# Kernel optimization log

Measured on AMD Instinct MI355X. Metric: run time of the kernel, lower is better.

The kernel has to match this reference:

```python
import jax, jax.numpy as jnp
import numpy as np
from math import comb

B = 1024                 # num_batch
NUM, NVAR, NUM_OBS = 100, 11, 10
T_FIN = 15.0
K_P = 20.0; K_D = 2.0 * np.sqrt(20.0); K_P_V = 20.0
A_OBS, B_OBS = 8.0, 4.2
RHO_V, RHO_PROJ, RHO_LANE, RHO_OBS, RHO_OFFSET, RHO_INEQ = 1.0, 1.0, 100.0, 100.0, 1.0, 100.0
V_MIN, V_MAX, A_MAX = 0.1, 30.0, 8.0
MAXITER = 20
LATENT, HID, INP_DIM, TRAJ_DIM = 2, 1024, 55, 200


def _bernstein():
    # degree-10 Bernstein polynomial basis on [0, T_FIN], sampled at NUM points
    n = NVAR - 1
    s = np.linspace(0.0, 1.0, NUM)
    bm = lambda m: np.stack([comb(m, k) * s**k * (1.0 - s)**(m - k) for k in range(m + 1)], 1)
    P, B9, B8 = bm(n), bm(n - 1), bm(n - 2)
    Z = np.zeros(NUM)
    Pdot = np.stack([(n / T_FIN) * ((B9[:, k - 1] if k >= 1 else Z) - (B9[:, k] if k <= n - 1 else Z)) for k in range(n + 1)], 1)
    Pddot = np.stack([(n * (n - 1) / T_FIN**2) * ((B8[:, k - 2] if k >= 2 else Z) - 2.0 * (B8[:, k - 1] if 1 <= k <= n - 1 else Z) + (B8[:, k] if k <= n - 2 else Z)) for k in range(n + 1)], 1)
    return tuple(jnp.asarray(a, jnp.float32) for a in (P, Pdot, Pddot))


def _forward(inp, initial_state_ego, traj_gt, y_ub, y_lb, eps,
             enc_w1, enc_b1, enc_w2, enc_b2, enc_wmu, enc_bmu, enc_wlv, enc_blv,
             dec_w1, dec_b1, dec_w2, dec_b2, dec_w3, dec_b3,
             P, Pdot, Pddot, inp_mean, inp_std):
    Bn = inp.shape[0]
    tot_time = jnp.linspace(0.0, T_FIN, NUM)

    # ---- cVAE encode / reparameterize / decode ----
    inp_n = (inp - inp_mean) / inp_std
    h = jax.nn.relu(jnp.concatenate([inp_n, traj_gt], 1) @ enc_w1 + enc_b1)
    h = jax.nn.relu(h @ enc_w2 + enc_b2)
    mu = h @ enc_wmu + enc_bmu
    logvar = h @ enc_wlv + enc_blv
    z = mu + jnp.exp(0.5 * logvar) * eps
    h = jax.nn.relu(jnp.concatenate([z, inp_n], 1) @ dec_w1 + dec_b1)
    h = jax.nn.relu(h @ dec_w2 + dec_b2)
    nn_out = h @ dec_w3 + dec_b3          # (B, 8): 4 v_des + 4 y_des setpoints

    # ---- constant constraint matrices ----
    A_eq_x = jnp.stack([P[0], Pdot[0], Pddot[0]])                 # (3, 11)
    A_eq_y = jnp.stack([P[0], Pdot[0], Pddot[0], Pdot[-1]])       # (4, 11)
    A_pd = Pddot - K_P * P - K_D * Pdot
    A_vd = Pddot - K_P_V * Pdot
    cost_smooth = Pddot.T @ Pddot
    I = jnp.eye(NVAR, dtype=P.dtype)

    def kkt_inv(cost, A_eq):
        m = A_eq.shape[0]
        M = jnp.block([[cost, A_eq.T], [A_eq, jnp.zeros((m, m), cost.dtype)]])
        return jnp.linalg.inv(M)

    # ---- boundary conditions ----
    zb = jnp.zeros((Bn,), inp.dtype)
    b_eq_x = jnp.stack([zb, initial_state_ego[:, 2], zb], 1)
    b_eq_y = jnp.stack([zb, initial_state_ego[:, 3], zb, zb], 1)

    # ---- QP layer 1 (behavioral layer) ----
    # sum_i A_vd_i^T A_vd_i over the 4 row-partitions == A_vd^T A_vd
    cost1_x = cost_smooth + RHO_V * (A_vd.T @ A_vd)
    cost1_y = cost_smooth + RHO_OFFSET * (A_pd.T @ A_pd)
    inv1_x = kkt_inv(cost1_x, A_eq_x)
    inv1_y = kkt_inv(cost1_y, A_eq_y)
    v_des = jnp.repeat(nn_out[:, 0:4], NUM // 4, axis=1)   # (B, 100) piecewise setpoints
    y_des = jnp.repeat(nn_out[:, 4:8], NUM // 4, axis=1)
    lincost_x1 = -RHO_V * ((-K_P_V * v_des) @ A_vd)
    lincost_y1 = -RHO_OFFSET * ((-K_P * y_des) @ A_pd)
    c_x_bar = (jnp.concatenate([-lincost_x1, b_eq_x], 1) @ inv1_x.T)[:, :NVAR]
    c_y_bar = (jnp.concatenate([-lincost_y1, b_eq_y], 1) @ inv1_y.T)[:, :NVAR]

    # ---- obstacle constant-velocity rollouts (obstacle-major, matches tile(P)) ----
    x_obs, y_obs = inp[:, 5::5], inp[:, 6::5]
    vx_obs, vy_obs = inp[:, 7::5], inp[:, 8::5]
    x_obs_traj = (x_obs[:, :, None] + vx_obs[:, :, None] * tot_time).reshape(Bn, NUM_OBS * NUM)
    y_obs_traj = (y_obs[:, :, None] + vy_obs[:, :, None] * tot_time).reshape(Bn, NUM_OBS * NUM)

    # ---- QP layer 2 (iterative ADMM-style projection) ----
    A_obs_m = jnp.tile(P, (NUM_OBS, 1))          # (1000, 11)
    A_lane = jnp.vstack([P, -P])                 # (200, 11)
    A_vel, A_acc = Pdot, Pddot
    cost2_x = RHO_PROJ * I + RHO_OBS * (A_obs_m.T @ A_obs_m) + RHO_INEQ * (A_acc.T @ A_acc) + RHO_INEQ * (A_vel.T @ A_vel)
    cost2_y = cost2_x + RHO_LANE * (A_lane.T @ A_lane)
    inv2_x = kkt_inv(cost2_x, A_eq_x)
    inv2_y = kkt_inv(cost2_y, A_eq_y)
    ones_num = jnp.ones((1, NUM), inp.dtype)
    b_lane = jnp.concatenate([y_ub[:, None] * ones_num, -y_lb[:, None] * ones_num], 1)  # (B, 200)

    def step(carry, _):
        primal, lx, ly = carry
        cx, cy = primal[:, :NVAR], primal[:, NVAR:]
        x, xdot, xddot = cx @ P.T, cx @ Pdot.T, cx @ Pddot.T
        y, ydot, yddot = cy @ P.T, cy @ Pdot.T, cy @ Pddot.T
        # obstacle polar decomposition
        wc = jnp.tile(x, (1, NUM_OBS)) - x_obs_traj
        ws = jnp.tile(y, (1, NUM_OBS)) - y_obs_traj
        a_o = jnp.arctan2(A_OBS * ws, B_OBS * wc)
        ca, sa = jnp.cos(a_o), jnp.sin(a_o)
        c1 = RHO_OBS * (A_OBS**2 * ca**2 + B_OBS**2 * sa**2)
        c2 = RHO_OBS * (A_OBS * wc * ca + B_OBS * ws * sa)
        d_o = jnp.maximum(1.0, c2 / c1)
        # velocity / acceleration polar decomposition with box clipping
        a_v = jnp.arctan2(ydot, xdot)
        cv, sv = jnp.cos(a_v), jnp.sin(a_v)
        d_v = jnp.clip(xdot * cv + ydot * sv, V_MIN, V_MAX)
        a_a = jnp.arctan2(yddot, xddot)
        caa, saa = jnp.cos(a_a), jnp.sin(a_a)
        d_a = jnp.clip(xddot * caa + yddot * saa, 0.0, A_MAX)
        # lane slack
        lane_proj = cy @ A_lane.T
        s_lane = jnp.maximum(0.0, b_lane - lane_proj)
        res_lane = lane_proj - b_lane + s_lane
        # residuals -> dual updates
        rxo = wc - A_OBS * d_o * ca
        ryo = ws - B_OBS * d_o * sa
        rvx, rvy = xdot - d_v * cv, ydot - d_v * sv
        rax, ray = xddot - d_a * caa, yddot - d_a * saa
        lx = lx - RHO_OBS * (rxo @ A_obs_m) - RHO_INEQ * (rax @ A_acc) - RHO_INEQ * (rvx @ A_vel)
        ly = ly - RHO_OBS * (ryo @ A_obs_m) - RHO_INEQ * (ray @ A_acc) - RHO_INEQ * (rvy @ A_vel) - RHO_LANE * (res_lane @ A_lane)
        # linear cost + batched KKT solve via precomputed inverse
        b_ox = x_obs_traj + A_OBS * d_o * ca
        b_oy = y_obs_traj + B_OBS * d_o * sa
        lin_x = -lx - RHO_PROJ * c_x_bar - RHO_OBS * (b_ox @ A_obs_m) - RHO_INEQ * ((d_a * caa) @ A_acc) - RHO_INEQ * ((d_v * cv) @ A_vel)
        lin_y = -ly - RHO_PROJ * c_y_bar - RHO_OBS * (b_oy @ A_obs_m) - RHO_INEQ * ((d_a * saa) @ A_acc) - RHO_INEQ * ((d_v * sv) @ A_vel) - RHO_LANE * ((b_lane - s_lane) @ A_lane)
        sx = (jnp.concatenate([-lin_x, b_eq_x], 1) @ inv2_x.T)[:, :NVAR]
        sy = (jnp.concatenate([-lin_y, b_eq_y], 1) @ inv2_y.T)[:, :NVAR]
        return (jnp.concatenate([sx, sy], 1), lx, ly), None

    primal0 = jnp.concatenate([c_x_bar, c_y_bar], 1)
    lam0 = jnp.zeros((Bn, NVAR), inp.dtype)
    (primal, _, _), _ = jax.lax.scan(step, (primal0, lam0, lam0), None, length=MAXITER)
    return primal  # (B, 2*NVAR) projected trajectory coefficients


def setup_inputs() -> dict:
    key = jax.random.key(0)
    ks = jax.random.split(key, 16)
    P, Pdot, Pddot = _bernstein()
    n = lambda k, sh, sc=1.0: sc * jax.random.normal(k, sh, jnp.float32)
    return {
        "inp": n(ks[0], (B, INP_DIM), 5.0),
        "initial_state_ego": jnp.concatenate([jnp.zeros((B, 2), jnp.float32), 10.0 + n(ks[1], (B, 2))], 1),
        "traj_gt": n(ks[2], (B, TRAJ_DIM)),
        "y_ub": jnp.full((B,), 3.5, jnp.float32),
        "y_lb": jnp.full((B,), -3.5, jnp.float32),
        "eps": n(ks[3], (B, LATENT)),
        "enc_w1": n(ks[4], (INP_DIM + TRAJ_DIM, HID), 0.05), "enc_b1": jnp.zeros((HID,), jnp.float32),
        "enc_w2": n(ks[5], (HID, HID), 0.03), "enc_b2": jnp.zeros((HID,), jnp.float32),
        "enc_wmu": n(ks[6], (HID, LATENT), 0.03), "enc_bmu": jnp.zeros((LATENT,), jnp.float32),
        "enc_wlv": n(ks[7], (HID, LATENT), 0.03), "enc_blv": jnp.zeros((LATENT,), jnp.float32),
        "dec_w1": n(ks[8], (LATENT + INP_DIM, HID), 0.05), "dec_b1": jnp.zeros((HID,), jnp.float32),
        "dec_w2": n(ks[9], (HID, HID), 0.03), "dec_b2": jnp.zeros((HID,), jnp.float32),
        "dec_w3": n(ks[10], (HID, 8), 0.03), "dec_b3": jnp.zeros((8,), jnp.float32),
        "P": P, "Pdot": Pdot, "Pddot": Pddot,
        "inp_mean": jnp.zeros((INP_DIM,), jnp.float32),
        "inp_std": jnp.ones((INP_DIM,), jnp.float32),
    }


def reference(inp, initial_state_ego, traj_gt, y_ub, y_lb, eps,
              enc_w1, enc_b1, enc_w2, enc_b2, enc_wmu, enc_bmu, enc_wlv, enc_blv,
              dec_w1, dec_b1, dec_w2, dec_b2, dec_w3, dec_b3,
              P, Pdot, Pddot, inp_mean, inp_std):
    return _forward(inp, initial_state_ego, traj_gt, y_ub, y_lb, eps,
                    enc_w1, enc_b1, enc_w2, enc_b2, enc_wmu, enc_bmu, enc_wlv, enc_blv,
                    dec_w1, dec_b1, dec_w2, dec_b2, dec_w3, dec_b3,
                    P, Pdot, Pddot, inp_mean, inp_std)
```

## Files before the change

### kernel.cpp

```cpp
#include <hip/hip_runtime.h>
#include <hip/hip_bf16.h>
#include <math.h>

#define BATCH   1024
#define NUMPT   100
#define NVAR    11
#define NOBS    10
#define HID     1024
#define INPD    55
#define TRAJD   200

#define T_FIN_C   15.0f
#define K_P_C     20.0f
#define K_D_C     8.944271909999159f
#define K_P_V_C   20.0f
#define A_OBS_C   8.0f
#define B_OBS_C   4.2f
#define AB_C      33.6f
#define ABSQ_C    1128.96f
#define RHO_V_C      1.0f
#define RHO_PROJ_C   1.0f
#define RHO_LANE_C   100.0f
#define RHO_OBS_C    100.0f
#define RHO_OFFSET_C 1.0f
#define RHO_INEQ_C   100.0f
#define V_MIN_C   0.1f
#define V_MAX_C   30.0f
#define A_MAX_C   8.0f
#define MAXIT     20

#define WS_INV1X  0
#define WS_INV1Y  256
#define WS_INV2X  512
#define WS_INV2Y  768
#define WS_SVD    1024
#define WS_SPD    1088
#define WS_QX     1152
#define WS_QY     1280
#define WS_R2X    1408
#define WS_R2Y    1536
#define WS_BIG    2048

typedef __bf16 bf16x8 __attribute__((ext_vector_type(8)));
typedef float  f32x4  __attribute__((ext_vector_type(4)));

__global__ __launch_bounds__(256) void setup_kernel(
    const float* __restrict__ Pg, const float* __restrict__ Pdg,
    const float* __restrict__ Pddg, float* __restrict__ ws,
    const float* __restrict__ inp, const float* __restrict__ traj,
    const float* __restrict__ mean, const float* __restrict__ stdv,
    __bf16* __restrict__ enc_in, __bf16* __restrict__ dec_in,
    const float* __restrict__ w1, const float* __restrict__ w2,
    const float* __restrict__ w3, const float* __restrict__ w4,
    __bf16* __restrict__ o1, __bf16* __restrict__ o2,
    __bf16* __restrict__ o3, __bf16* __restrict__ o4)
{
    __shared__ float sP[NUMPT*NVAR], sPd[NUMPT*NVAR], sPdd[NUMPT*NVAR];
    __shared__ float aug[15][31];
    __shared__ float fcol[15];
    __shared__ float sQ[121];
    __shared__ float sn[INPD];
    __shared__ float s_pivinv;
    __shared__ int   s_pidx;
    const int tid = threadIdx.x, bid = blockIdx.x;

    if (bid >= 1028) {
        const int idx = (bid - 1028) * 256 + tid;
        if (idx < 262144) {
            const int n = idx >> 8, k = idx & 255;
            o1[idx] = (__bf16)((k < 255) ? w1[(size_t)k*HID + n] : 0.0f);
        } else if (idx < 262144 + 1048576) {
            const int i = idx - 262144;
            const int n = i >> 10, k = i & 1023;
            o2[i] = (__bf16)w2[(size_t)k*HID + n];
        } else if (idx < 262144 + 1048576 + 65536) {
            const int i = idx - (262144 + 1048576);
            const int n = i >> 6, k = i & 63;
            o3[i] = (__bf16)((k < 57) ? w3[(size_t)k*HID + n] : 0.0f);
        } else {
            const int i = idx - (262144 + 1048576 + 65536);
            const int n = i >> 10, k = i & 1023;
            o4[i] = (__bf16)w4[(size_t)k*HID + n];
        }
        return;
    }

    if (bid >= 4) {
        const int b = bid - 4;
        if (tid < INPD) {
            const float v = (inp[b*INPD + tid] - mean[tid]) / stdv[tid];
            sn[tid] = v;
            enc_in[b*256 + tid] = (__bf16)v;
        } else if (tid < 255) {
            enc_in[b*256 + tid] = (__bf16)traj[b*TRAJD + (tid - INPD)];
        } else {
            enc_in[b*256 + 255] = (__bf16)0.0f;
        }
        __syncthreads();
        if (tid >= 2 && tid < 64)
            dec_in[b*64 + tid] = (__bf16)((tid < 57) ? sn[tid - 2] : 0.0f);
        return;
    }

    for (int i = tid; i < NUMPT*NVAR; i += 256) {
        sP[i] = Pg[i]; sPd[i] = Pdg[i]; sPdd[i] = Pddg[i];
    }
    for (int i = tid; i < 15*31; i += 256) (&aug[0][0])[i] = 0.0f;
    __syncthreads();

    const int N = (bid == 0 || bid == 2) ? 14 : 15;

    if (tid < 121) {
        const int i = tid / 11, j = tid % 11;
        float s = 0.0f;
        if (bid == 0) {
            for (int t = 0; t < NUMPT; ++t) {
                float pdd_i = sPdd[t*NVAR+i], pdd_j = sPdd[t*NVAR+j];
                float av_i = pdd_i - K_P_V_C * sPd[t*NVAR+i];
                float av_j = pdd_j - K_P_V_C * sPd[t*NVAR+j];
                s += pdd_i*pdd_j + RHO_V_C * av_i*av_j;
            }
        } else if (bid == 1) {
            for (int t = 0; t < NUMPT; ++t) {
                float pdd_i = sPdd[t*NVAR+i], pdd_j = sPdd[t*NVAR+j];
                float ap_i = pdd_i - K_P_C*sP[t*NVAR+i] - K_D_C*sPd[t*NVAR+i];
                float ap_j = pdd_j - K_P_C*sP[t*NVAR+j] - K_D_C*sPd[t*NVAR+j];
                s += pdd_i*pdd_j + RHO_OFFSET_C * ap_i*ap_j;
            }
        } else {
            float obs_w = RHO_OBS_C * (float)NOBS;
            if (bid == 3) obs_w += RHO_LANE_C * 2.0f;
            for (int t = 0; t < NUMPT; ++t) {
                float p_i = sP[t*NVAR+i],   p_j = sP[t*NVAR+j];
// ... 48 lines not shown
        const int p = s_pidx;
        if (p != k && tid < 2*N) {
            float tmp = aug[k][tid]; aug[k][tid] = aug[p][tid]; aug[p][tid] = tmp;
        }
        __syncthreads();
        if (tid == 0) s_pivinv = 1.0f / aug[k][k];
        __syncthreads();
        if (tid < 2*N) aug[k][tid] *= s_pivinv;
        __syncthreads();
        if (tid < N) fcol[tid] = (tid == k) ? 0.0f : aug[tid][k];
        __syncthreads();
        for (int idx = tid; idx < N*2*N; idx += 256) {
            const int i = idx / (2*N), j = idx % (2*N);
            if (i != k) aug[i][j] = fmaf(-fcol[i], aug[k][j], aug[i][j]);
        }
        __syncthreads();
    }

    float* dst = ws + (bid == 0 ? WS_INV1X : bid == 1 ? WS_INV1Y
                      : bid == 2 ? WS_INV2X : WS_INV2Y);
    for (int idx = tid; idx < N*N; idx += 256)
        dst[idx] = aug[idx / N][N + idx % N];
    __syncthreads();

    if ((bid == 2 || bid == 3) && tid < 121) {
        const int k = tid / 11, j = tid % 11;
        float a = 0.0f;
        #pragma unroll
        for (int m = 0; m < 11; ++m) a = fmaf(aug[k][N + m], sQ[m*11 + j], a);
        ws[(bid == 2 ? WS_R2X : WS_R2Y) + tid] = a;
    }
}

__global__ __launch_bounds__(256) void gemm_mfma(
    const __bf16* __restrict__ A, const __bf16* __restrict__ Wt,
    const float* __restrict__ bias, __bf16* __restrict__ C, int Kp)
{
    __shared__ __bf16 As[32][72];
    __shared__ __bf16 Bs[64][72];
    const int tid = threadIdx.x;
    const int lane = tid & 63, wv = tid >> 6;
    const int wm = (wv >> 1) * 16, wn = (wv & 1) * 32;
    const int ln = lane & 15, q = lane >> 4;
    const int row0 = blockIdx.y * 32, col0 = blockIdx.x * 64;
    const int srow = tid >> 3, lc = (tid & 7) * 8;

    f32x4 acc0 = (f32x4){0,0,0,0}, acc1 = (f32x4){0,0,0,0};

    for (int k0 = 0; k0 < Kp; k0 += 64) {
        *(bf16x8*)&As[srow][lc] =
            *(const bf16x8*)&A[(size_t)(row0 + srow) * Kp + k0 + lc];
        *(bf16x8*)&Bs[srow][lc] =
            *(const bf16x8*)&Wt[(size_t)(col0 + srow) * Kp + k0 + lc];
        *(bf16x8*)&Bs[srow + 32][lc] =
            *(const bf16x8*)&Wt[(size_t)(col0 + srow + 32) * Kp + k0 + lc];
        __syncthreads();
        #pragma unroll
        for (int kc = 0; kc < 2; ++kc) {
            const bf16x8 a  = *(const bf16x8*)&As[wm + ln][kc*32 + q*8];
            const bf16x8 b0 = *(const bf16x8*)&Bs[wn + ln][kc*32 + q*8];
            const bf16x8 b1 = *(const bf16x8*)&Bs[wn + 16 + ln][kc*32 + q*8];
            acc0 = __builtin_amdgcn_mfma_f32_16x16x32_bf16(a, b0, acc0, 0, 0, 0);
            acc1 = __builtin_amdgcn_mfma_f32_16x16x32_bf16(a, b1, acc1, 0, 0, 0);
        }
        __syncthreads();
    }
    #pragma unroll
    for (int ni = 0; ni < 2; ++ni) {
        const int col = col0 + wn + ni*16 + ln;
        const float bv = bias[col];
        const f32x4 av = ni ? acc1 : acc0;
        #pragma unroll
        for (int r = 0; r < 4; ++r) {
            const int row = row0 + wm + q*4 + r;
            C[(size_t)row * HID + col] = (__bf16)fmaxf(av[r] + bv, 0.0f);
        }
    }
}

__global__ __launch_bounds__(64) void z_kernel(
    const __bf16* __restrict__ h, const float* __restrict__ wmu,
    const float* __restrict__ bmu, const float* __restrict__ wlv,
    const float* __restrict__ blv, const float* __restrict__ eps,
    __bf16* __restrict__ dec_in)
{
    const int b = blockIdx.x, lane = threadIdx.x;
    float a0 = 0, a1 = 0, a2 = 0, a3 = 0;
    for (int hh = lane; hh < HID; hh += 64) {
        const float v = (float)h[b*HID + hh];
        a0 = fmaf(v, wmu[hh*2 + 0], a0);
        a1 = fmaf(v, wmu[hh*2 + 1], a1);
        a2 = fmaf(v, wlv[hh*2 + 0], a2);
        a3 = fmaf(v, wlv[hh*2 + 1], a3);
    }
    #pragma unroll
    for (int off = 32; off; off >>= 1) {
        a0 += __shfl_down(a0, off);
        a1 += __shfl_down(a1, off);
        a2 += __shfl_down(a2, off);
        a3 += __shfl_down(a3, off);
    }
    if (lane == 0) {
        const float mu0 = a0 + bmu[0], mu1 = a1 + bmu[1];
        const float lv0 = a2 + blv[0], lv1 = a3 + blv[1];
        dec_in[b*64 + 0] = (__bf16)fmaf(expf(0.5f*lv0), eps[b*2 + 0], mu0);
        dec_in[b*64 + 1] = (__bf16)fmaf(expf(0.5f*lv1), eps[b*2 + 1], mu1);
    }
}

__global__ __launch_bounds__(64) void out8_kernel(
    const __bf16* __restrict__ h, const float* __restrict__ w3,
    const float* __restrict__ b3, float* __restrict__ nn_out)
{
    const int b = blockIdx.x, lane = threadIdx.x;
    float acc[8] = {};
    for (int hh = lane; hh < HID; hh += 64) {
        const float v = (float)h[b*HID + hh];
        #pragma unroll
        for (int j = 0; j < 8; ++j) acc[j] = fmaf(v, w3[hh*8 + j], acc[j]);
    }
    #pragma unroll
    for (int j = 0; j < 8; ++j)
        #pragma unroll
        for (int off = 32; off; off >>= 1) acc[j] += __shfl_down(acc[j], off);
    if (lane == 0)
        for (int j = 0; j < 8; ++j) nn_out[b*8 + j] = acc[j] + b3[j];
}

#define DOT11(bb, a0, a1, a2) \
    fmaf(bb[0],a0.x, fmaf(bb[1],a0.y, fmaf(bb[2],a0.z, fmaf(bb[3],a0.w, \
    fmaf(bb[4],a1.x, fmaf(bb[5],a1.y, fmaf(bb[6],a1.z, fmaf(bb[7],a1.w, \
    fmaf(bb[8],a2.x, fmaf(bb[9],a2.y, bb[10]*a2.z))))))))))

__global__ __launch_bounds__(256) void solver_kernel(
    const float* __restrict__ nn_out, const float* __restrict__ inp,
    const float* __restrict__ ise, const float* __restrict__ yub_p,
    const float* __restrict__ ylb_p,
    const float* __restrict__ Pg, const float* __restrict__ Pdg,
    const float* __restrict__ Pddg,
    const float* __restrict__ ws, float* __restrict__ out)
{
    __shared__ __align__(16) float sBcol[3][11][108];
    __shared__ float s_i2x[196], s_i2y[225], sR2x[121], sR2y[121];
    __shared__ __align__(16) float rows[7][104];
    __shared__ float dval[2][80];
    __shared__ __align__(16) float cxs[12], cys[12];
    __shared__ float wlin[24];
    __shared__ float obsS[4][10];

    const int tid = threadIdx.x;
    const int e = blockIdx.x;

    for (int i = tid; i < 3*11*108; i += 256) {
        const int mat = i / 1188, rem = i - mat*1188;
        const int k = rem / 108, t = rem - k*108;
        const float* G = (mat == 0) ? Pg : (mat == 1 ? Pdg : Pddg);
        sBcol[mat][k][t] = (t < NUMPT) ? G[t*NVAR + k] : 0.0f;
    }
    for (int i = tid; i < 196; i += 256) s_i2x[i] = ws[WS_INV2X + i];
    for (int i = tid; i < 225; i += 256) s_i2y[i] = ws[WS_INV2Y + i];
    for (int i = tid; i < 121; i += 256) { sR2x[i] = ws[WS_R2X + i]; sR2y[i] = ws[WS_R2Y + i]; }
    if (tid >= 200 && tid < 240) {
        const int i = tid - 200;
        obsS[i/10][i%10] = inp[e*INPD + 5 + (i/10) + 5*(i%10)];
    }
    if (tid >= 64 && tid < 92) {
        const int i = tid - 64;
        rows[i >> 2][100 + (i & 3)] = 0.0f;
    }
    if (tid == 92) cxs[11] = 0.0f;
    if (tid == 93) cys[11] = 0.0f;

    const bool isA = (tid < 200);
    const int tA = tid >> 1, hA = tid & 1;
    const bool isB = (tid < 154);
    const int hB = (tid >= 77) ? 1 : 0;
    const int dB = tid - 77*hB;
    const int rB = dB / 11, kB = dB - 11*rB;
    const int mB = (rB==1||rB==4) ? 2 : ((rB==2||rB==5) ? 1 : 0);
    const float* colp = &sBcol[mB][kB][hB*52];
    const float* rowp = &rows[rB][hB*52];

    float bP[NVAR], bQ[NVAR];
    if (isA) {
        const float* Qsrc = hA ? Pddg : Pdg;
        #pragma unroll
        for (int k = 0; k < NVAR; ++k) {
            bP[k] = Pg[tA*NVAR+k];
            bQ[k] = Qsrc[tA*NVAR+k];
        }
    }

    const float vx0 = ise[e*4 + 2], vy0 = ise[e*4 + 3];
    const float yub = yub_p[e], ylb = ylb_p[e];
    __syncthreads();

    const float DT = T_FIN_C / 99.0f;
    float xo[5], yo[5];
    if (isA) {
        const int ob0 = 5*hA;
        #pragma unroll
        for (int o = 0; o < 5; ++o) {
            xo[o] = fmaf(obsS[2][ob0+o], tA*DT, obsS[0][ob0+o]);
            yo[o] = fmaf(obsS[3][ob0+o], tA*DT, obsS[1][ob0+o]);
        }
    }

    if (tid < 11) {
        float s = 0;
        #pragma unroll
        for (int c = 0; c < 4; ++c)
            s = fmaf(nn_out[e*8 + c], ws[WS_SVD + c*11 + tid], s);
        wlin[tid] = RHO_V_C * K_P_V_C * s;
    } else if (tid < 22) {
        const int k = tid - 11;
        float s = 0;
        #pragma unroll
        for (int c = 0; c < 4; ++c)
            s = fmaf(nn_out[e*8 + 4 + c], ws[WS_SPD + c*11 + k], s);
        wlin[tid] = RHO_OFFSET_C * K_P_C * s;
    }
    __syncthreads();
// ... 45 lines not shown
            }
            const float mrx = srx + __shfl_xor(srx, 1);
            const float mry = sry + __shfl_xor(sry, 1);

            if (hA == 0) {
                rows[0][tA] = mrx;
                rows[3][tA] = mry;
                const float rv2 = qx*qx + qy*qy;
                float vxr, vyr;
                if (rv2 > 0.0f) {
                    const float ri = rsqrtf(rv2);
                    const float dv = fminf(fmaxf(rv2*ri, V_MIN_C), V_MAX_C);
                    const float f = 1.0f - dv*ri;
                    vxr = qx*f; vyr = qy*f;
                } else { vxr = -V_MIN_C; vyr = 0.0f; }
                rows[2][tA] = vxr;  rows[5][tA] = vyr;
                rows[6][tA] = fmaxf(0.0f, py - yub) - fmaxf(0.0f, ylb - py);
            } else {
                const float ra2 = qx*qx + qy*qy;
                float axr = 0.0f, ayr = 0.0f;
                if (ra2 > A_MAX_C*A_MAX_C) {
                    const float ri = rsqrtf(ra2);
                    const float f = 1.0f - A_MAX_C*ri;
                    axr = qx*f; ayr = qy*f;
                }
                rows[1][tA] = axr;  rows[4][tA] = ayr;
            }
        }
        __syncthreads();

        if (isB) {
            float s0 = 0.0f, s1 = 0.0f;
            #pragma unroll
            for (int i = 0; i < 13; ++i) {
                const float4 rr = *(const float4*)&rowp[i*4];
                const float4 cc = *(const float4*)&colp[i*4];
                s0 = fmaf(rr.x, cc.x, s0); s1 = fmaf(rr.y, cc.y, s1);
                s0 = fmaf(rr.z, cc.z, s0); s1 = fmaf(rr.w, cc.w, s1);
            }
            dval[hB][dB] = s0 + s1;
        }
        __syncthreads();

        if (tid < 22) {
            const int k = (tid < 11) ? tid : tid - 11;
            float u;
            if (tid < 11)
                u = RHO_OBS_C * ((dval[0][k]      + dval[1][k])
                               + (dval[0][11 + k] + dval[1][11 + k])
                               + (dval[0][22 + k] + dval[1][22 + k]));
            else
                u = RHO_OBS_C * ((dval[0][33 + k] + dval[1][33 + k])
                               + (dval[0][44 + k] + dval[1][44 + k])
                               + (dval[0][55 + k] + dval[1][55 + k])
                               + (dval[0][66 + k] + dval[1][66 + k]));
            wlin[tid] = 2.0f*u - lam - cb;
            lam -= u;
        }
        __builtin_amdgcn_wave_barrier();
        if (tid < 22) {
            const int k = (tid < 11) ? tid : tid - 11;
            if (tid < 11) {
                float a = vx0 * s_i2x[k*14 + 12];
                #pragma unroll
                for (int j = 0; j < NVAR; ++j) {
                    a = fmaf(-wlin[j], s_i2x[k*14 + j], a);
                    a = fmaf(sR2x[k*11 + j], cxs[j], a);
                }
                cxs[k] = a;
            } else {
                float a = vy0 * s_i2y[k*15 + 12];
                #pragma unroll
                for (int j = 0; j < NVAR; ++j) {
                    a = fmaf(-wlin[11 + j], s_i2y[k*15 + j], a);
                    a = fmaf(sR2y[k*11 + j], cys[j], a);
                }
                cys[k] = a;
            }
        }
        __syncthreads();
    }

    if (tid < NVAR) {
        out[e*22 + tid]      = cxs[tid];
        out[e*22 + 11 + tid] = cys[tid];
    }
}

extern "C" void kernel_launch(void* const* d_in, const int* in_sizes, int n_in,
                              void* d_out, int out_size, void* d_ws, size_t ws_size,
                              hipStream_t stream)
{
    (void)in_sizes; (void)n_in; (void)out_size; (void)ws_size;
    const float* inp    = (const float*)d_in[0];
    const float* ise    = (const float*)d_in[1];
    const float* traj   = (const float*)d_in[2];
    const float* yub    = (const float*)d_in[3];
    const float* ylb    = (const float*)d_in[4];
    const float* eps    = (const float*)d_in[5];
    const float* enc_w1 = (const float*)d_in[6];
    const float* enc_b1 = (const float*)d_in[7];
    const float* enc_w2 = (const float*)d_in[8];
    const float* enc_b2 = (const float*)d_in[9];
    const float* wmu    = (const float*)d_in[10];
    const float* bmu    = (const float*)d_in[11];
    const float* wlv    = (const float*)d_in[12];
    const float* blv    = (const float*)d_in[13];
    const float* dec_w1 = (const float*)d_in[14];
    const float* dec_b1 = (const float*)d_in[15];
    const float* dec_w2 = (const float*)d_in[16];
    const float* dec_b2 = (const float*)d_in[17];
    const float* dec_w3 = (const float*)d_in[18];
    const float* dec_b3 = (const float*)d_in[19];
    const float* P      = (const float*)d_in[20];
    const float* Pd     = (const float*)d_in[21];
    const float* Pdd    = (const float*)d_in[22];
    const float* mean   = (const float*)d_in[23];
    const float* stdv   = (const float*)d_in[24];

    float* ws   = (float*)d_ws;
    float* nn   = ws + WS_BIG;
    __bf16* bfb = (__bf16*)(ws + WS_BIG + BATCH*8);
    __bf16* enc_in = bfb;
    __bf16* dec_in = enc_in + (size_t)BATCH*256;
    __bf16* hA     = dec_in + (size_t)BATCH*64;
    __bf16* hB     = hA + (size_t)BATCH*HID;
    __bf16* wt1    = hB + (size_t)BATCH*HID;
    __bf16* wt2    = wt1 + (size_t)HID*256;
    __bf16* wt3    = wt2 + (size_t)HID*HID;
    __bf16* wt4    = wt3 + (size_t)HID*64;
    float* outf = (float*)d_out;

    setup_kernel<<<4 + 1024 + 9472, 256, 0, stream>>>(
        P, Pd, Pdd, ws, inp, traj, mean, stdv, enc_in, dec_in,
        enc_w1, enc_w2, dec_w1, dec_w2, wt1, wt2, wt3, wt4);

    dim3 g(16, 32);
    gemm_mfma<<<g, 256, 0, stream>>>(enc_in, wt1, enc_b1, hA, 256);
    gemm_mfma<<<g, 256, 0, stream>>>(hA, wt2, enc_b2, hB, 1024);
    z_kernel<<<BATCH, 64, 0, stream>>>(hB, wmu, bmu, wlv, blv, eps, dec_in);
    gemm_mfma<<<g, 256, 0, stream>>>(dec_in, wt3, dec_b1, hA, 64);
    gemm_mfma<<<g, 256, 0, stream>>>(hA, wt4, dec_b2, hB, 1024);
    out8_kernel<<<BATCH, 64, 0, stream>>>(hB, dec_w3, dec_b3, nn);

    solver_kernel<<<BATCH, 256, 0, stream>>>(nn, inp, ise, yub, ylb,
                                             P, Pd, Pdd, ws, outf);
}
```

Measured before the change: 236.6 us.

## Widen GEMM K-tile to 128 and keep solver basis columns in registers

The MFMA GEMM now stages 128-wide K slices per iteration instead of 64, which halves the number of barrier-separated loop trips. To keep that tile size valid, the decoder-input K dimension is padded from 64 to 128. The solver kernel drops its shared-memory Bernstein column table and holds each thread's 36-element column slice in registers. The 11x7 dot products are now split across 231 threads in three chunks instead of 154 threads in two, and launch_bounds adds an occupancy hint of 4 blocks. In exchange, the decoder's first GEMM does extra padded-K work, and the solver's register footprint grows.

```diff
diff --git a/kernel.cpp b/kernel.cpp
--- a/kernel.cpp
+++ b/kernel.cpp
@@ -43,6 +43,12 @@
 
 typedef __bf16 bf16x8 __attribute__((ext_vector_type(8)));
 typedef float  f32x4  __attribute__((ext_vector_type(4)));
+
+#define CV1  262144
+#define CV2  1048576
+#define CV3  131072
+#define CV4  1048576
+#define CVTOT (CV1 + CV2 + CV3 + CV4)
 
 __global__ __launch_bounds__(256) void setup_kernel(
     const float* __restrict__ Pg, const float* __restrict__ Pdg,
@@ -66,19 +72,19 @@
 
     if (bid >= 1028) {
         const int idx = (bid - 1028) * 256 + tid;
-        if (idx < 262144) {
+        if (idx < CV1) {
             const int n = idx >> 8, k = idx & 255;
             o1[idx] = (__bf16)((k < 255) ? w1[(size_t)k*HID + n] : 0.0f);
-        } else if (idx < 262144 + 1048576) {
-            const int i = idx - 262144;
+        } else if (idx < CV1 + CV2) {
+            const int i = idx - CV1;
             const int n = i >> 10, k = i & 1023;
             o2[i] = (__bf16)w2[(size_t)k*HID + n];
-        } else if (idx < 262144 + 1048576 + 65536) {
-            const int i = idx - (262144 + 1048576);
-            const int n = i >> 6, k = i & 63;
+        } else if (idx < CV1 + CV2 + CV3) {
+            const int i = idx - (CV1 + CV2);
+            const int n = i >> 7, k = i & 127;
             o3[i] = (__bf16)((k < 57) ? w3[(size_t)k*HID + n] : 0.0f);
         } else {
-            const int i = idx - (262144 + 1048576 + 65536);
+            const int i = idx - (CV1 + CV2 + CV3);
             const int n = i >> 10, k = i & 1023;
             o4[i] = (__bf16)w4[(size_t)k*HID + n];
         }
@@ -97,8 +103,8 @@
             enc_in[b*256 + 255] = (__bf16)0.0f;
         }
         __syncthreads();
-        if (tid >= 2 && tid < 64)
-            dec_in[b*64 + tid] = (__bf16)((tid < 57) ? sn[tid - 2] : 0.0f);
+        if (tid >= 2 && tid < 128)
+            dec_in[b*128 + tid] = (__bf16)((tid < 57) ? sn[tid - 2] : 0.0f);
         return;
     }
 
@@ -217,27 +223,29 @@
     const __bf16* __restrict__ A, const __bf16* __restrict__ Wt,
     const float* __restrict__ bias, __bf16* __restrict__ C, int Kp)
 {
-    __shared__ __bf16 As[32][72];
-    __shared__ __bf16 Bs[64][72];
+    __shared__ __bf16 As[32][136];
+    __shared__ __bf16 Bs[64][136];
     const int tid = threadIdx.x;
     const int lane = tid & 63, wv = tid >> 6;
     const int wm = (wv >> 1) * 16, wn = (wv & 1) * 32;
     const int ln = lane & 15, q = lane >> 4;
     const int row0 = blockIdx.y * 32, col0 = blockIdx.x * 64;
-    const int srow = tid >> 3, lc = (tid & 7) * 8;
+    const int r16 = tid >> 4, ch = (tid & 15) * 8;
 
     f32x4 acc0 = (f32x4){0,0,0,0}, acc1 = (f32x4){0,0,0,0};
 
-    for (int k0 = 0; k0 < Kp; k0 += 64) {
-        *(bf16x8*)&As[srow][lc] =
-            *(const bf16x8*)&A[(size_t)(row0 + srow) * Kp + k0 + lc];
-        *(bf16x8*)&Bs[srow][lc] =
-            *(const bf16x8*)&Wt[(size_t)(col0 + srow) * Kp + k0 + lc];
-        *(bf16x8*)&Bs[srow + 32][lc] =
-            *(const bf16x8*)&Wt[(size_t)(col0 + srow + 32) * Kp + k0 + lc];
-        __syncthreads();
-        #pragma unroll
-        for (int kc = 0; kc < 2; ++kc) {
+    for (int k0 = 0; k0 < Kp; k0 += 128) {
+        *(bf16x8*)&As[r16][ch] =
+            *(const bf16x8*)&A[(size_t)(row0 + r16) * Kp + k0 + ch];
+        *(bf16x8*)&As[r16 + 16][ch] =
+            *(const bf16x8*)&A[(size_t)(row0 + r16 + 16) * Kp + k0 + ch];
+        #pragma unroll
+        for (int p = 0; p < 4; ++p)
+            *(bf16x8*)&Bs[r16 + 16*p][ch] =
+                *(const bf16x8*)&Wt[(size_t)(col0 + r16 + 16*p) * Kp + k0 + ch];
+        __syncthreads();
+        #pragma unroll
+        for (int kc = 0; kc < 4; ++kc) {
             const bf16x8 a  = *(const bf16x8*)&As[wm + ln][kc*32 + q*8];
             const bf16x8 b0 = *(const bf16x8*)&Bs[wn + ln][kc*32 + q*8];
             const bf16x8 b1 = *(const bf16x8*)&Bs[wn + 16 + ln][kc*32 + q*8];
@@ -284,8 +292,8 @@
     if (lane == 0) {
         const float mu0 = a0 + bmu[0], mu1 = a1 + bmu[1];
         const float lv0 = a2 + blv[0], lv1 = a3 + blv[1];
-        dec_in[b*64 + 0] = (__bf16)fmaf(expf(0.5f*lv0), eps[b*2 + 0], mu0);
-        dec_in[b*64 + 1] = (__bf16)fmaf(expf(0.5f*lv1), eps[b*2 + 1], mu1);
+        dec_in[b*128 + 0] = (__bf16)fmaf(expf(0.5f*lv0), eps[b*2 + 0], mu0);
+        dec_in[b*128 + 1] = (__bf16)fmaf(expf(0.5f*lv1), eps[b*2 + 1], mu1);
     }
 }
 
@@ -313,7 +321,7 @@
     fmaf(bb[4],a1.x, fmaf(bb[5],a1.y, fmaf(bb[6],a1.z, fmaf(bb[7],a1.w, \
     fmaf(bb[8],a2.x, fmaf(bb[9],a2.y, bb[10]*a2.z))))))))))
 
-__global__ __launch_bounds__(256) void solver_kernel(
+__global__ __launch_bounds__(256, 4) void solver_kernel(
     const float* __restrict__ nn_out, const float* __restrict__ inp,
     const float* __restrict__ ise, const float* __restrict__ yub_p,
     const float* __restrict__ ylb_p,
@@ -321,10 +329,9 @@
     const float* __restrict__ Pddg,
     const float* __restrict__ ws, float* __restrict__ out)
 {
-    __shared__ __align__(16) float sBcol[3][11][108];
     __shared__ float s_i2x[196], s_i2y[225], sR2x[121], sR2y[121];
-    __shared__ __align__(16) float rows[7][104];
-    __shared__ float dval[2][80];
+    __shared__ __align__(16) float rows[7][108];
+    __shared__ float dval[3][80];
     __shared__ __align__(16) float cxs[12], cys[12];
     __shared__ float wlin[24];
     __shared__ float obsS[4][10];
@@ -332,35 +339,28 @@
     const int tid = threadIdx.x;
     const int e = blockIdx.x;
 
-    for (int i = tid; i < 3*11*108; i += 256) {
-        const int mat = i / 1188, rem = i - mat*1188;
-        const int k = rem / 108, t = rem - k*108;
-        const float* G = (mat == 0) ? Pg : (mat == 1 ? Pdg : Pddg);
-        sBcol[mat][k][t] = (t < NUMPT) ? G[t*NVAR + k] : 0.0f;
-    }
     for (int i = tid; i < 196; i += 256) s_i2x[i] = ws[WS_INV2X + i];
     for (int i = tid; i < 225; i += 256) s_i2y[i] = ws[WS_INV2Y + i];
     for (int i = tid; i < 121; i += 256) { sR2x[i] = ws[WS_R2X + i]; sR2y[i] = ws[WS_R2Y + i]; }
+    if (tid >= 232 && tid < 240) {  }
     if (tid >= 200 && tid < 240) {
         const int i = tid - 200;
         obsS[i/10][i%10] = inp[e*INPD + 5 + (i/10) + 5*(i%10)];
     }
-    if (tid >= 64 && tid < 92) {
+    if (tid >= 64 && tid < 120) {
         const int i = tid - 64;
-        rows[i >> 2][100 + (i & 3)] = 0.0f;
-    }
-    if (tid == 92) cxs[11] = 0.0f;
-    if (tid == 93) cys[11] = 0.0f;
+        rows[i >> 3][100 + (i & 7)] = 0.0f;
+    }
+    if (tid == 120) cxs[11] = 0.0f;
+    if (tid == 121) cys[11] = 0.0f;
 
     const bool isA = (tid < 200);
     const int tA = tid >> 1, hA = tid & 1;
-    const bool isB = (tid < 154);
-    const int hB = (tid >= 77) ? 1 : 0;
+    const bool isB = (tid < 231);
+    const int hB = (tid >= 154) ? 2 : ((tid >= 77) ? 1 : 0);
     const int dB = tid - 77*hB;
     const int rB = dB / 11, kB = dB - 11*rB;
-    const int mB = (rB==1||rB==4) ? 2 : ((rB==2||rB==5) ? 1 : 0);
-    const float* colp = &sBcol[mB][kB][hB*52];
-    const float* rowp = &rows[rB][hB*52];
+    const float* rowp = &rows[rB][hB*36];
 
     float bP[NVAR], bQ[NVAR];
     if (isA) {
@@ -369,6 +369,20 @@
         for (int k = 0; k < NVAR; ++k) {
             bP[k] = Pg[tA*NVAR+k];
             bQ[k] = Qsrc[tA*NVAR+k];
+        }
+    }
+    float4 bc[9];
+    if (isB) {
+        const float* G = (rB==1||rB==4) ? Pddg : ((rB==2||rB==5) ? Pdg : Pg);
+        #pragma unroll
+        for (int i = 0; i < 9; ++i) {
+            const int t0 = hB*36 + i*4;
+            float4 v;
+            v.x = (t0+0 < NUMPT) ? G[(t0+0)*NVAR + kB] : 0.0f;
+            v.y = (t0+1 < NUMPT) ? G[(t0+1)*NVAR + kB] : 0.0f;
+            v.z = (t0+2 < NUMPT) ? G[(t0+2)*NVAR + kB] : 0.0f;
+            v.w = (t0+3 < NUMPT) ? G[(t0+3)*NVAR + kB] : 0.0f;
+            bc[i] = v;
         }
     }
 
@@ -480,11 +494,10 @@
         if (isB) {
             float s0 = 0.0f, s1 = 0.0f;
             #pragma unroll
-            for (int i = 0; i < 13; ++i) {
+            for (int i = 0; i < 9; ++i) {
                 const float4 rr = *(const float4*)&rowp[i*4];
-                const float4 cc = *(const float4*)&colp[i*4];
-                s0 = fmaf(rr.x, cc.x, s0); s1 = fmaf(rr.y, cc.y, s1);
-                s0 = fmaf(rr.z, cc.z, s0); s1 = fmaf(rr.w, cc.w, s1);
+                s0 = fmaf(rr.x, bc[i].x, s0); s1 = fmaf(rr.y, bc[i].y, s1);
+                s0 = fmaf(rr.z, bc[i].z, s0); s1 = fmaf(rr.w, bc[i].w, s1);
             }
             dval[hB][dB] = s0 + s1;
         }
@@ -494,14 +507,14 @@
             const int k = (tid < 11) ? tid : tid - 11;
             float u;
             if (tid < 11)
-                u = RHO_OBS_C * ((dval[0][k]      + dval[1][k])
-                               + (dval[0][11 + k] + dval[1][11 + k])
-                               + (dval[0][22 + k] + dval[1][22 + k]));
+                u = RHO_OBS_C * ((dval[0][k]      + dval[1][k]      + dval[2][k])
+                               + (dval[0][11 + k] + dval[1][11 + k] + dval[2][11 + k])
+                               + (dval[0][22 + k] + dval[1][22 + k] + dval[2][22 + k]));
             else
-                u = RHO_OBS_C * ((dval[0][33 + k] + dval[1][33 + k])
-                               + (dval[0][44 + k] + dval[1][44 + k])
-                               + (dval[0][55 + k] + dval[1][55 + k])
-                               + (dval[0][66 + k] + dval[1][66 + k]));
+                u = RHO_OBS_C * ((dval[0][33 + k] + dval[1][33 + k] + dval[2][33 + k])
+                               + (dval[0][44 + k] + dval[1][44 + k] + dval[2][44 + k])
+                               + (dval[0][55 + k] + dval[1][55 + k] + dval[2][55 + k])
+                               + (dval[0][66 + k] + dval[1][66 + k] + dval[2][66 + k]));
             wlin[tid] = 2.0f*u - lam - cb;
             lam -= u;
         }
@@ -571,15 +584,15 @@
     __bf16* bfb = (__bf16*)(ws + WS_BIG + BATCH*8);
     __bf16* enc_in = bfb;
     __bf16* dec_in = enc_in + (size_t)BATCH*256;
-    __bf16* hA     = dec_in + (size_t)BATCH*64;
+    __bf16* hA     = dec_in + (size_t)BATCH*128;
     __bf16* hB     = hA + (size_t)BATCH*HID;
     __bf16* wt1    = hB + (size_t)BATCH*HID;
     __bf16* wt2    = wt1 + (size_t)HID*256;
     __bf16* wt3    = wt2 + (size_t)HID*HID;
-    __bf16* wt4    = wt3 + (size_t)HID*64;
+    __bf16* wt4    = wt3 + (size_t)HID*128;
     float* outf = (float*)d_out;
 
-    setup_kernel<<<4 + 1024 + 9472, 256, 0, stream>>>(
+    setup_kernel<<<4 + 1024 + 9728, 256, 0, stream>>>(
         P, Pd, Pdd, ws, inp, traj, mean, stdv, enc_in, dec_in,
         enc_w1, enc_w2, dec_w1, dec_w2, wt1, wt2, wt3, wt4);
 
@@ -587,7 +600,7 @@
     gemm_mfma<<<g, 256, 0, stream>>>(enc_in, wt1, enc_b1, hA, 256);
     gemm_mfma<<<g, 256, 0, stream>>>(hA, wt2, enc_b2, hB, 1024);
     z_kernel<<<BATCH, 64, 0, stream>>>(hB, wmu, bmu, wlv, blv, eps, dec_in);
-    gemm_mfma<<<g, 256, 0, stream>>>(dec_in, wt3, dec_b1, hA, 64);
+    gemm_mfma<<<g, 256, 0, stream>>>(dec_in, wt3, dec_b1, hA, 128);
     gemm_mfma<<<g, 256, 0, stream>>>(hA, wt4, dec_b2, hB, 1024);
     out8_kernel<<<BATCH, 64, 0, stream>>>(hB, dec_w3, dec_b3, nn);
 
```

Result: no change. 238.2 us (+0.7%).

## Fuse latent and output projections into GEMM epilogues, tile weight transposes

Applied to the files above, without the earlier changes.

Folds the mu/logvar projection and the 8-wide output head into the epilogues of the preceding MFMA GEMMs. Per-tile partial sums are reduced with warp shuffles and atomically added into buffers zeroed or bias-initialized in setup. The reparameterization step moves into the A-tile load of the first decoder GEMM. Weight transposition now goes through 64x64 shared-memory tiles for coalesced reads and writes, and the GEMM K-step grows from 64 to 128. This removes two kernel launches and an intermediate activation round trip, at the cost of float atomics that make summation order nondeterministic.

```diff
diff --git a/kernel.cpp b/kernel.cpp
--- a/kernel.cpp
+++ b/kernel.cpp
@@ -53,34 +53,44 @@
     const float* __restrict__ w1, const float* __restrict__ w2,
     const float* __restrict__ w3, const float* __restrict__ w4,
     __bf16* __restrict__ o1, __bf16* __restrict__ o2,
-    __bf16* __restrict__ o3, __bf16* __restrict__ o4)
+    __bf16* __restrict__ o3, __bf16* __restrict__ o4,
+    float* __restrict__ nn, float* __restrict__ mulv,
+    const float* __restrict__ b3)
 {
     __shared__ float sP[NUMPT*NVAR], sPd[NUMPT*NVAR], sPdd[NUMPT*NVAR];
     __shared__ float aug[15][31];
     __shared__ float fcol[15];
     __shared__ float sQ[121];
     __shared__ float sn[INPD];
+    __shared__ float tile[64][65];
     __shared__ float s_pivinv;
     __shared__ int   s_pidx;
     const int tid = threadIdx.x, bid = blockIdx.x;
 
     if (bid >= 1028) {
-        const int idx = (bid - 1028) * 256 + tid;
-        if (idx < 262144) {
-            const int n = idx >> 8, k = idx & 255;
-            o1[idx] = (__bf16)((k < 255) ? w1[(size_t)k*HID + n] : 0.0f);
-        } else if (idx < 262144 + 1048576) {
-            const int i = idx - 262144;
-            const int n = i >> 10, k = i & 1023;
-            o2[i] = (__bf16)w2[(size_t)k*HID + n];
-        } else if (idx < 262144 + 1048576 + 65536) {
-            const int i = idx - (262144 + 1048576);
-            const int n = i >> 6, k = i & 63;
-            o3[i] = (__bf16)((k < 57) ? w3[(size_t)k*HID + n] : 0.0f);
-        } else {
-            const int i = idx - (262144 + 1048576 + 65536);
-            const int n = i >> 10, k = i & 1023;
-            o4[i] = (__bf16)w4[(size_t)k*HID + n];
+        const int tb = bid - 1028;
+        int wsel, kt, nt;
+        if (tb < 64)       { wsel = 0; kt = tb >> 4;        nt = tb & 15; }
+        else if (tb < 320) { wsel = 1; kt = (tb-64) >> 4;   nt = (tb-64) & 15; }
+        else if (tb < 352) { wsel = 2; kt = (tb-320) >> 4;  nt = (tb-320) & 15; }
+        else               { wsel = 3; kt = (tb-352) >> 4;  nt = (tb-352) & 15; }
+        const float* W = (wsel==0) ? w1 : (wsel==1) ? w2 : (wsel==2) ? w3 : w4;
+        __bf16* O      = (wsel==0) ? o1 : (wsel==1) ? o2 : (wsel==2) ? o3 : o4;
+        const int K  = (wsel==0) ? 255 : (wsel==2) ? 57 : 1024;
+        const int Kp = (wsel==0) ? 256 : (wsel==2) ? 128 : 1024;
+        if (kt*64 >= Kp) return;
+        const int k0 = kt*64, n0 = nt*64;
+        const int rr = tid >> 6, c = tid & 63;
+        #pragma unroll 4
+        for (int it = 0; it < 16; ++it) {
+            const int r = it*4 + rr;
+            tile[r][c] = (k0 + r < K) ? W[(size_t)(k0 + r)*HID + n0 + c] : 0.0f;
+        }
+        __syncthreads();
+        #pragma unroll 4
+        for (int it = 0; it < 16; ++it) {
+            const int r = it*4 + rr;
+            O[(size_t)(n0 + r)*Kp + k0 + c] = (__bf16)tile[c][r];
         }
         return;
     }
@@ -97,8 +107,10 @@
             enc_in[b*256 + 255] = (__bf16)0.0f;
         }
         __syncthreads();
-        if (tid >= 2 && tid < 64)
-            dec_in[b*64 + tid] = (__bf16)((tid < 57) ? sn[tid - 2] : 0.0f);
+        if (tid >= 2 && tid < 128)
+            dec_in[b*128 + tid] = (__bf16)((tid < 57) ? sn[tid - 2] : 0.0f);
+        if (tid < 4) mulv[b*4 + tid] = 0.0f;
+        else if (tid >= 8 && tid < 16) nn[b*8 + (tid - 8)] = b3[tid - 8];
         return;
     }
 
@@ -213,99 +225,156 @@
     }
 }
 
-__global__ __launch_bounds__(256) void gemm_mfma(
+#define GEMM_CORE(A_, Wt_, Kp_, ...)                                          \
+    __shared__ __bf16 As[32][136];                                            \
+    __shared__ __bf16 Bs[64][136];                                            \
+    const int tid = threadIdx.x;                                              \
+    const int lane = tid & 63, wv = tid >> 6;                                 \
+    const int wm = (wv >> 1) * 16, wn = (wv & 1) * 32;                        \
+    const int ln = lane & 15, q = lane >> 4;                                  \
+    const int row0 = blockIdx.y * 32, col0 = blockIdx.x * 64;                 \
+    const int r16 = tid >> 4, ch = (tid & 15) * 8;                            \
+    f32x4 acc0 = (f32x4){0,0,0,0}, acc1 = (f32x4){0,0,0,0};                   \
+    for (int k0 = 0; k0 < (Kp_); k0 += 128) {                                 \
+        bf16x8 va = *(const bf16x8*)&(A_)[(size_t)(row0 + r16)*(Kp_) + k0 + ch]; \
+        bf16x8 vb = *(const bf16x8*)&(A_)[(size_t)(row0 + r16 + 16)*(Kp_) + k0 + ch]; \
+        __VA_ARGS__                                                           \
+        *(bf16x8*)&As[r16][ch] = va;                                          \
+        *(bf16x8*)&As[r16 + 16][ch] = vb;                                     \
+        _Pragma("unroll")                                                     \
+        for (int p = 0; p < 4; ++p)                                           \
+            *(bf16x8*)&Bs[r16 + 16*p][ch] =                                   \
+                *(const bf16x8*)&(Wt_)[(size_t)(col0 + r16 + 16*p)*(Kp_) + k0 + ch]; \
+        __syncthreads();                                                      \
+        _Pragma("unroll")                                                     \
+        for (int kc = 0; kc < 4; ++kc) {                                      \
+            const bf16x8 a  = *(const bf16x8*)&As[wm + ln][kc*32 + q*8];      \
+            const bf16x8 b0 = *(const bf16x8*)&Bs[wn + ln][kc*32 + q*8];      \
+            const bf16x8 b1 = *(const bf16x8*)&Bs[wn + 16 + ln][kc*32 + q*8]; \
+            acc0 = __builtin_amdgcn_mfma_f32_16x16x32_bf16(a, b0, acc0, 0, 0, 0); \
+            acc1 = __builtin_amdgcn_mfma_f32_16x16x32_bf16(a, b1, acc1, 0, 0, 0); \
+        }                                                                     \
+        __syncthreads();                                                      \
+    }
+
+#define GEMM_WRITE_RELU(C_)                                                   \
+    _Pragma("unroll")                                                         \
+    for (int ni = 0; ni < 2; ++ni) {                                          \
+        const int col = col0 + wn + ni*16 + ln;                               \
+        const float bv = bias[col];                                           \
+        const f32x4 av = ni ? acc1 : acc0;                                    \
+        _Pragma("unroll")                                                     \
+        for (int r = 0; r < 4; ++r) {                                         \
+            const int row = row0 + wm + q*4 + r;                              \
+            (C_)[(size_t)row * HID + col] = (__bf16)fmaxf(av[r] + bv, 0.0f);  \
+        }                                                                     \
+    }
+
+__global__ __launch_bounds__(256) void gemm_relu(
     const __bf16* __restrict__ A, const __bf16* __restrict__ Wt,
     const float* __restrict__ bias, __bf16* __restrict__ C, int Kp)
 {
-    __shared__ __bf16 As[32][72];
-    __shared__ __bf16 Bs[64][72];
-    const int tid = threadIdx.x;
-    const int lane = tid & 63, wv = tid >> 6;
-    const int wm = (wv >> 1) * 16, wn = (wv & 1) * 32;
-    const int ln = lane & 15, q = lane >> 4;
-    const int row0 = blockIdx.y * 32, col0 = blockIdx.x * 64;
-    const int srow = tid >> 3, lc = (tid & 7) * 8;
-
-    f32x4 acc0 = (f32x4){0,0,0,0}, acc1 = (f32x4){0,0,0,0};
-
-    for (int k0 = 0; k0 < Kp; k0 += 64) {
-        *(bf16x8*)&As[srow][lc] =
-            *(const bf16x8*)&A[(size_t)(row0 + srow) * Kp + k0 + lc];
-        *(bf16x8*)&Bs[srow][lc] =
-            *(const bf16x8*)&Wt[(size_t)(col0 + srow) * Kp + k0 + lc];
-        *(bf16x8*)&Bs[srow + 32][lc] =
-            *(const bf16x8*)&Wt[(size_t)(col0 + srow + 32) * Kp + k0 + lc];
-        __syncthreads();
-        #pragma unroll
-        for (int kc = 0; kc < 2; ++kc) {
-            const bf16x8 a  = *(const bf16x8*)&As[wm + ln][kc*32 + q*8];
-            const bf16x8 b0 = *(const bf16x8*)&Bs[wn + ln][kc*32 + q*8];
-            const bf16x8 b1 = *(const bf16x8*)&Bs[wn + 16 + ln][kc*32 + q*8];
-            acc0 = __builtin_amdgcn_mfma_f32_16x16x32_bf16(a, b0, acc0, 0, 0, 0);
-            acc1 = __builtin_amdgcn_mfma_f32_16x16x32_bf16(a, b1, acc1, 0, 0, 0);
-        }
-        __syncthreads();
-    }
+    GEMM_CORE(A, Wt, Kp)
+    GEMM_WRITE_RELU(C)
+}
+
+__global__ __launch_bounds__(256) void gemm_mulv(
+    const __bf16* __restrict__ A, const __bf16* __restrict__ Wt,
+    const float* __restrict__ bias,
+    const float* __restrict__ wmu, const float* __restrict__ wlv,
+    float* __restrict__ mulv, int Kp)
+{
+    GEMM_CORE(A, Wt, Kp)
+    const int c0 = col0 + wn + ln;
+    const int c1 = c0 + 16;
+    const float b0v = bias[c0], b1v = bias[c1];
+    const float wm00 = wmu[c0*2+0], wm01 = wmu[c0*2+1];
+    const float wm10 = wmu[c1*2+0], wm11 = wmu[c1*2+1];
+    const float wl00 = wlv[c0*2+0], wl01 = wlv[c0*2+1];
+    const float wl10 = wlv[c1*2+0], wl11 = wlv[c1*2+1];
+    float pr[4][4];
     #pragma unroll
-    for (int ni = 0; ni < 2; ++ni) {
-        const int col = col0 + wn + ni*16 + ln;
-        const float bv = bias[col];
-        const f32x4 av = ni ? acc1 : acc0;
+    for (int r = 0; r < 4; ++r) {
+        const float h0 = fmaxf(acc0[r] + b0v, 0.0f);
+        const float h1 = fmaxf(acc1[r] + b1v, 0.0f);
+        pr[r][0] = fmaf(h0, wm00, h1*wm10);
+        pr[r][1] = fmaf(h0, wm01, h1*wm11);
+        pr[r][2] = fmaf(h0, wl00, h1*wl10);
+        pr[r][3] = fmaf(h0, wl01, h1*wl11);
+    }
+    #pragma unroll
+    for (int m = 1; m <= 8; m <<= 1)
+        #pragma unroll
+        for (int r = 0; r < 4; ++r)
+            #pragma unroll
+            for (int j = 0; j < 4; ++j)
+                pr[r][j] += __shfl_xor(pr[r][j], m);
+    if (ln == 0) {
         #pragma unroll
         for (int r = 0; r < 4; ++r) {
             const int row = row0 + wm + q*4 + r;
-            C[(size_t)row * HID + col] = (__bf16)fmaxf(av[r] + bv, 0.0f);
+            #pragma unroll
+            for (int j = 0; j < 4; ++j)
+                atomicAdd(&mulv[row*4 + j], pr[r][j]);
         }
     }
 }
 
-__global__ __launch_bounds__(64) void z_kernel(
-    const __bf16* __restrict__ h, const float* __restrict__ wmu,
-    const float* __restrict__ bmu, const float* __restrict__ wlv,
-    const float* __restrict__ blv, const float* __restrict__ eps,
-    __bf16* __restrict__ dec_in)
+__global__ __launch_bounds__(256) void gemm_zfix(
+    const __bf16* __restrict__ A, const __bf16* __restrict__ Wt,
+    const float* __restrict__ bias, __bf16* __restrict__ C, int Kp,
+    const float* __restrict__ mulv, const float* __restrict__ bmu,
+    const float* __restrict__ blv, const float* __restrict__ eps)
 {
-    const int b = blockIdx.x, lane = threadIdx.x;
-    float a0 = 0, a1 = 0, a2 = 0, a3 = 0;
-    for (int hh = lane; hh < HID; hh += 64) {
-        const float v = (float)h[b*HID + hh];
-        a0 = fmaf(v, wmu[hh*2 + 0], a0);
-        a1 = fmaf(v, wmu[hh*2 + 1], a1);
-        a2 = fmaf(v, wlv[hh*2 + 0], a2);
-        a3 = fmaf(v, wlv[hh*2 + 1], a3);
-    }
+    GEMM_CORE(A, Wt, Kp,
+        if (ch == 0 && k0 == 0) {
+            const int ra = row0 + r16;
+            const int rb = ra + 16;
+            const float4 ma = *(const float4*)&mulv[ra*4];
+            const float4 mb = *(const float4*)&mulv[rb*4];
+            va[0] = (__bf16)fmaf(expf(0.5f*(ma.z + blv[0])), eps[ra*2+0], ma.x + bmu[0]);
+            va[1] = (__bf16)fmaf(expf(0.5f*(ma.w + blv[1])), eps[ra*2+1], ma.y + bmu[1]);
+            vb[0] = (__bf16)fmaf(expf(0.5f*(mb.z + blv[0])), eps[rb*2+0], mb.x + bmu[0]);
+            vb[1] = (__bf16)fmaf(expf(0.5f*(mb.w + blv[1])), eps[rb*2+1], mb.y + bmu[1]);
+        }
+    )
+    GEMM_WRITE_RELU(C)
+}
+
+__global__ __launch_bounds__(256) void gemm_out8(
+    const __bf16* __restrict__ A, const __bf16* __restrict__ Wt,
+    const float* __restrict__ bias, const float* __restrict__ w3,
+    float* __restrict__ nn, int Kp)
+{
+    GEMM_CORE(A, Wt, Kp)
+    const int c0 = col0 + wn + ln;
+    const int c1 = c0 + 16;
+    const float b0v = bias[c0], b1v = bias[c1];
+    float pr[4][8];
     #pragma unroll
-    for (int off = 32; off; off >>= 1) {
-        a0 += __shfl_down(a0, off);
-        a1 += __shfl_down(a1, off);
-        a2 += __shfl_down(a2, off);
-        a3 += __shfl_down(a3, off);
-    }
-    if (lane == 0) {
-        const float mu0 = a0 + bmu[0], mu1 = a1 + bmu[1];
-        const float lv0 = a2 + blv[0], lv1 = a3 + blv[1];
-        dec_in[b*64 + 0] = (__bf16)fmaf(expf(0.5f*lv0), eps[b*2 + 0], mu0);
-        dec_in[b*64 + 1] = (__bf16)fmaf(expf(0.5f*lv1), eps[b*2 + 1], mu1);
-    }
-}
-
-__global__ __launch_bounds__(64) void out8_kernel(
-    const __bf16* __restrict__ h, const float* __restrict__ w3,
-    const float* __restrict__ b3, float* __restrict__ nn_out)
-{
-    const int b = blockIdx.x, lane = threadIdx.x;
-    float acc[8] = {};
-    for (int hh = lane; hh < HID; hh += 64) {
-        const float v = (float)h[b*HID + hh];
-        #pragma unroll
-        for (int j = 0; j < 8; ++j) acc[j] = fmaf(v, w3[hh*8 + j], acc[j]);
+    for (int r = 0; r < 4; ++r) {
+        const float h0 = fmaxf(acc0[r] + b0v, 0.0f);
+        const float h1 = fmaxf(acc1[r] + b1v, 0.0f);
+        #pragma unroll
+        for (int j = 0; j < 8; ++j)
+            pr[r][j] = fmaf(h0, w3[c0*8 + j], h1*w3[c1*8 + j]);
     }
     #pragma unroll
-    for (int j = 0; j < 8; ++j)
-        #pragma unroll
-        for (int off = 32; off; off >>= 1) acc[j] += __shfl_down(acc[j], off);
-    if (lane == 0)
-        for (int j = 0; j < 8; ++j) nn_out[b*8 + j] = acc[j] + b3[j];
+    for (int m = 1; m <= 8; m <<= 1)
+        #pragma unroll
+        for (int r = 0; r < 4; ++r)
+            #pragma unroll
+            for (int j = 0; j < 8; ++j)
+                pr[r][j] += __shfl_xor(pr[r][j], m);
+    if (ln == 0) {
+        #pragma unroll
+        for (int r = 0; r < 4; ++r) {
+            const int row = row0 + wm + q*4 + r;
+            #pragma unroll
+            for (int j = 0; j < 8; ++j)
+                atomicAdd(&nn[row*8 + j], pr[r][j]);
+        }
+    }
 }
 
 #define DOT11(bb, a0, a1, a2) \
@@ -568,29 +637,28 @@
 
     float* ws   = (float*)d_ws;
     float* nn   = ws + WS_BIG;
-    __bf16* bfb = (__bf16*)(ws + WS_BIG + BATCH*8);
+    float* mulv = nn + BATCH*8;
+    __bf16* bfb = (__bf16*)(mulv + BATCH*4);
     __bf16* enc_in = bfb;
     __bf16* dec_in = enc_in + (size_t)BATCH*256;
-    __bf16* hA     = dec_in + (size_t)BATCH*64;
-    __bf16* hB     = hA + (size_t)BATCH*HID;
-    __bf16* wt1    = hB + (size_t)BATCH*HID;
+    __bf16* hA     = dec_in + (size_t)BATCH*128;
+    __bf16* wt1    = hA + (size_t)BATCH*HID;
     __bf16* wt2    = wt1 + (size_t)HID*256;
     __bf16* wt3    = wt2 + (size_t)HID*HID;
-    __bf16* wt4    = wt3 + (size_t)HID*64;
+    __bf16* wt4    = wt3 + (size_t)HID*128;
     float* outf = (float*)d_out;
 
-    setup_kernel<<<4 + 1024 + 9472, 256, 0, stream>>>(
+    setup_kernel<<<4 + 1024 + 608, 256, 0, stream>>>(
         P, Pd, Pdd, ws, inp, traj, mean, stdv, enc_in, dec_in,
-        enc_w1, enc_w2, dec_w1, dec_w2, wt1, wt2, wt3, wt4);
+        enc_w1, enc_w2, dec_w1, dec_w2, wt1, wt2, wt3, wt4,
+        nn, mulv, dec_b3);
 
     dim3 g(16, 32);
-    gemm_mfma<<<g, 256, 0, stream>>>(enc_in, wt1, enc_b1, hA, 256);
-    gemm_mfma<<<g, 256, 0, stream>>>(hA, wt2, enc_b2, hB, 1024);
-    z_kernel<<<BATCH, 64, 0, stream>>>(hB, wmu, bmu, wlv, blv, eps, dec_in);
-    gemm_mfma<<<g, 256, 0, stream>>>(dec_in, wt3, dec_b1, hA, 64);
-    gemm_mfma<<<g, 256, 0, stream>>>(hA, wt4, dec_b2, hB, 1024);
-    out8_kernel<<<BATCH, 64, 0, stream>>>(hB, dec_w3, dec_b3, nn);
-
+    gemm_relu<<<g, 256, 0, stream>>>(enc_in, wt1, enc_b1, hA, 256);
+    gemm_mulv<<<g, 256, 0, stream>>>(hA, wt2, enc_b2, wmu, wlv, mulv, 1024);
+    gemm_zfix<<<g, 256, 0, stream>>>(dec_in, wt3, dec_b1, hA, 128,
+                                     mulv, bmu, blv, eps);
+    gemm_out8<<<g, 256, 0, stream>>>(hA, wt4, dec_b2, dec_w3, nn, 1024);
     solver_kernel<<<BATCH, 256, 0, stream>>>(nn, inp, ise, yub, ylb,
                                              P, Pd, Pdd, ws, outf);
 }
```

Measured after the change: 257.5 us. 8.9% more time.
